# Optimization experiments

Measured on AMD Instinct MI355X. Metric: run time of the kernel, lower is better.

The kernel has to match this reference:

```python
import jax, jax.numpy as jnp
import numpy as np

C = 64  # channels fixed by module

def conv1x1(x, W, b):
    # x: [B,C,H,W], W: [C_out,C_in], b: [C_out]
    return jnp.einsum('bchw,oc->bohw', x, W) + b[None, :, None, None]

def setup_inputs() -> dict:
    key = jax.random.key(0)
    ks = jax.random.split(key, 16)
    B, H, W = 4, 64, 64
    inp = {
        'x_latter': jax.random.normal(ks[0], (B, C, H, W), jnp.float32),
        'x': jax.random.normal(ks[1], (B, C, H, W), jnp.float32),
    }
    scale = 1.0 / np.sqrt(C)
    names = ['high', 'low', 'value', 'e_conv', 'mid', 'latter']
    for i, n in enumerate(names):
        inp[f'W_{n}'] = jax.random.normal(ks[2 + 2 * i], (C, C), jnp.float32) * scale
        inp[f'b_{n}'] = jax.random.normal(ks[3 + 2 * i], (C,), jnp.float32) * 0.01
    return inp

def reference(x_latter, x, W_high, b_high, W_low, b_low, W_value, b_value,
              W_e_conv, b_e_conv, W_mid, b_mid, W_latter, b_latter):
    b, c, h, w = x_latter.shape
    hw = h * w
    # stage 1: channel-normalized spatial attention
    xl_hi = conv1x1(x_latter, W_high, b_high).reshape(b, c, hw)          # [b,c,hw]
    x_low = conv1x1(x, W_low, b_low).reshape(b, c, hw).transpose(0, 2, 1)  # [b,hw,c]
    p = jnp.einsum('bnc,bcm->bnm', x_low, xl_hi)                          # [b,hw,hw]
    p = jax.nn.softmax(p, axis=1)  # torch Softmax(dim=1) over first hw axis
    v = conv1x1(x, W_value, b_value).reshape(b, c, hw).transpose(0, 2, 1)  # [b,hw,c]
    e = jnp.einsum('bnm,bmc->bnc', p, v) + x_low                          # [b,hw,c]
    e = e.transpose(0, 2, 1).reshape(b, c, h, w)                          # [b,c,h,w]
    e = conv1x1(e, W_e_conv, b_e_conv).reshape(b, c, hw)                  # [b,c,hw]
    # stage 2: channel-channel attention
    xl2 = conv1x1(x_latter, W_latter, b_latter).reshape(b, c, hw).transpose(0, 2, 1)  # [b,hw,c]
    t = jnp.einsum('bcn,bnd->bcd', e, xl2)                                # [b,c,c]
    t = jax.nn.softmax(t, axis=1)
    x_mid = conv1x1(x, W_mid, b_mid).reshape(b, c, hw).transpose(0, 2, 1)  # [b,hw,c]
    out = jnp.einsum('bnc,bcd->bnd', x_mid, t)                            # [b,hw,c]
    return out.transpose(0, 2, 1).reshape(b, c, h, w)
```

## Files before the change

kernel.cpp:

```cpp
#include <hip/hip_runtime.h>
#include <math.h>

#define BATCH 4
#define CH 64
#define HW 4096

typedef __attribute__((ext_vector_type(8))) short short8;
typedef __attribute__((ext_vector_type(4))) float f32x4;
typedef __attribute__((ext_vector_type(4))) float float4v;

#define MFMA(a, b, c) __builtin_amdgcn_mfma_f32_16x16x32_bf16(a, b, c, 0, 0, 0)

__device__ __forceinline__ short f2bf(float f) {
    unsigned u = __builtin_bit_cast(unsigned, f);
    u += 0x7fffu + ((u >> 16) & 1u);
    return (short)(u >> 16);
}
__device__ __forceinline__ float bf2f(short s) {
    unsigned u = ((unsigned)(unsigned short)s) << 16;
    return __builtin_bit_cast(float, u);
}
__device__ __forceinline__ void gld16(const short* g, short* l) {
    __builtin_amdgcn_global_load_lds(
        (const __attribute__((address_space(1))) unsigned int*)g,
        (__attribute__((address_space(3))) unsigned int*)l, 16, 0, 0);
}

__global__ __launch_bounds__(256) void splitX(
    const float* __restrict__ x, const float* __restrict__ xl,
    short* __restrict__ XFh, short* __restrict__ XFl)
{
    int src = blockIdx.z, b = blockIdx.y, bx = blockIdx.x;
    const float* X = src ? xl : x;
    int t = threadIdx.x, wv = t >> 6, ln = t & 63;
    int nt = bx * 4 + wv;
    int n = (nt << 4) + (ln & 15);
    int g = ln >> 4;
    size_t sb = ((size_t)(src * BATCH + b) * 256 + nt) * 2;
    #pragma unroll
    for (int kt = 0; kt < 2; kt++) {
        short8 h, l;
        #pragma unroll
        for (int j = 0; j < 8; j++) {
            float v = X[(size_t)(b * 64 + kt * 32 + g * 8 + j) * HW + n];
            short hh = f2bf(v);
            h[j] = hh;
            l[j] = f2bf(v - bf2f(hh));
        }
        *(short8*)(XFh + (sb + kt) * 512 + (size_t)ln * 8) = h;
        *(short8*)(XFl + (sb + kt) * 512 + (size_t)ln * 8) = l;
    }
}

__global__ __launch_bounds__(256) void convm(
    const short* __restrict__ XFh, const short* __restrict__ XFl,
    const float* __restrict__ Wlow, const float* __restrict__ blow,
    const float* __restrict__ Wval, const float* __restrict__ bval,
    const float* __restrict__ Wmid, const float* __restrict__ bmid,
    const float* __restrict__ Wlat, const float* __restrict__ blat,
    const float* __restrict__ Whigh, const float* __restrict__ bhigh,
    float* __restrict__ XLOW, float* __restrict__ XMID, float* __restrict__ XL2,
    short* __restrict__ PAh, short* __restrict__ PAl,
    short* __restrict__ PBh, short* __restrict__ PBl,
    short* __restrict__ PVh, short* __restrict__ PVl)
{
    int mode = blockIdx.z, b = blockIdx.y, bx = blockIdx.x;
    const float* W; const float* bias; int src;
    switch (mode) {
        case 0:  W = Wlow;  bias = blow;  src = 0; break;
        case 1:  W = Wval;  bias = bval;  src = 0; break;
        case 2:  W = Wmid;  bias = bmid;  src = 0; break;
        case 3:  W = Wlat;  bias = blat;  src = 1; break;
        default: W = Whigh; bias = bhigh; src = 1; break;
    }
    int t = threadIdx.x, wv = t >> 6, ln = t & 63;
    int row = ln & 15, g = ln >> 4;

    short8 Wh[4][2], Wlo[4][2];
    #pragma unroll
    for (int ot = 0; ot < 4; ot++)
        #pragma unroll
        for (int kt = 0; kt < 2; kt++) {
            const float* wp = W + (ot * 16 + row) * 64 + kt * 32 + g * 8;
            short8 h, l;
            #pragma unroll
            for (int j = 0; j < 8; j++) {
                float v = wp[j];
                short hh = f2bf(v);
                h[j] = hh;
                l[j] = f2bf(v - bf2f(hh));
            }
            Wh[ot][kt] = h; Wlo[ot][kt] = l;
        }

    int nt = bx * 4 + wv;
    size_t xb = ((size_t)(src * BATCH + b) * 256 + nt) * 2;
    short8 Bh[2], Bl[2];
    #pragma unroll
    for (int kt = 0; kt < 2; kt++) {
        Bh[kt] = *(const short8*)(XFh + (xb + kt) * 512 + (size_t)ln * 8);
        Bl[kt] = *(const short8*)(XFl + (xb + kt) * 512 + (size_t)ln * 8);
    }

    f32x4 acc[4];
    #pragma unroll
    for (int ot = 0; ot < 4; ot++) {
        #pragma unroll
        for (int r = 0; r < 4; r++) acc[ot][r] = bias[ot * 16 + g * 4 + r];
    }
    #pragma unroll
    for (int ot = 0; ot < 4; ot++)
        #pragma unroll
        for (int kt = 0; kt < 2; kt++) {
            acc[ot] = MFMA(Wh[ot][kt], Bh[kt], acc[ot]);
            acc[ot] = MFMA(Wh[ot][kt], Bl[kt], acc[ot]);
            acc[ot] = MFMA(Wlo[ot][kt], Bh[kt], acc[ot]);
        }

    __shared__ float Ld[64][65];
    #pragma unroll
    for (int ot = 0; ot < 4; ot++)
        #pragma unroll
        for (int r = 0; r < 4; r++)
            Ld[wv * 16 + (ln & 15)][ot * 16 + g * 4 + r] = acc[ot][r];
    __syncthreads();

    int n0 = bx * 64;
    if (mode == 0 || mode == 2 || mode == 3) {
        float* outp = (mode == 0) ? XLOW : (mode == 2) ? XMID : XL2;
        int n = t >> 2, o0 = (t & 3) * 16;
        float vout[16];
        #pragma unroll
        for (int k = 0; k < 16; k++) vout[k] = Ld[n][o0 + k];
        float* gp = outp + ((size_t)b * HW + n0 + n) * 64 + o0;
        #pragma unroll
        for (int k = 0; k < 4; k++)
            *(float4v*)(gp + k * 4) = *(float4v*)(vout + k * 4);
    }
    if (mode == 0 || mode == 4) {
        short* Ph = (mode == 0) ? PAh : PBh;
        short* Pl = (mode == 0) ? PAl : PBl;
        #pragma unroll
        for (int kt = 0; kt < 2; kt++) {
            short8 h, l;
            #pragma unroll
            for (int j = 0; j < 8; j++) {
                float v = Ld[wv * 16 + (ln & 15)][kt * 32 + g * 8 + j];
                short hh = f2bf(v);
                h[j] = hh;
                l[j] = f2bf(v - bf2f(hh));
            }
            size_t blob = (((size_t)b * 256 + bx * 4 + wv) * 2 + kt) * 512 + (size_t)ln * 8;
            *(short8*)(Ph + blob) = h;
            *(short8*)(Pl + blob) = l;
        }
    }
    if (mode == 1) {
        int ktm_l = wv >> 1;
        int ct0 = (wv & 1) * 2;
        #pragma unroll
        for (int cc = 0; cc < 2; cc++) {
            int ct = ct0 + cc;
            int c = ct * 16 + (ln & 15);
            short8 h, l;
            #pragma unroll
            for (int j = 0; j < 8; j++) {
                float v = Ld[ktm_l * 32 + g * 8 + j][c];
                short hh = f2bf(v);
                h[j] = hh;
                l[j] = f2bf(v - bf2f(hh));
            }
            size_t blob = (((size_t)b * 128 + bx * 2 + ktm_l) * 4 + ct) * 512 + (size_t)ln * 8;
            *(short8*)(PVh + blob) = h;
            *(short8*)(PVl + blob) = l;
        }
    }
}

__global__ __launch_bounds__(256) void zpass(
    const short* __restrict__ PAh, const short* __restrict__ PAl,
    const short* __restrict__ PBh, const short* __restrict__ PBl,
    float* __restrict__ Zp)
{
    int b = blockIdx.z, nc = blockIdx.y, mchunk = blockIdx.x;
    int t = threadIdx.x, wv = t >> 6, ln = t & 63;
    short8 bh[4][2], bl[4][2];
    #pragma unroll
    for (int msub = 0; msub < 4; msub++)
        #pragma unroll
        for (int kt = 0; kt < 2; kt++) {
            size_t o = ((size_t)(b * 256 + mchunk * 4 + msub) * 2 + kt) * 512 + ln * 8;
            bh[msub][kt] = *(const short8*)(PBh + o);
            bl[msub][kt] = *(const short8*)(PBl + o);
        }
    float zacc[4] = {0.f, 0.f, 0.f, 0.f};
    for (int s = 0; s < 16; s++) {
        int nt = nc * 64 + s * 4 + wv;
        size_t ab = ((size_t)(b * 256 + nt) * 2) * 512 + ln * 8;
        short8 ah0 = *(const short8*)(PAh + ab);
        short8 ah1 = *(const short8*)(PAh + ab + 512);
        short8 al0 = *(const short8*)(PAl + ab);
        short8 al1 = *(const short8*)(PAl + ab + 512);
        #pragma unroll
        for (int msub = 0; msub < 4; msub++) {
            f32x4 acc = {0.f, 0.f, 0.f, 0.f};
            acc = MFMA(ah0, bh[msub][0], acc);
            acc = MFMA(ah1, bh[msub][1], acc);
            acc = MFMA(ah0, bl[msub][0], acc);
            acc = MFMA(ah1, bl[msub][1], acc);
            acc = MFMA(al0, bh[msub][0], acc);
            acc = MFMA(al1, bh[msub][1], acc);
            float z = __expf(acc[0]) + __expf(acc[1]) + __expf(acc[2]) + __expf(acc[3]);
            z += __shfl_xor(z, 16, 64);
            z += __shfl_xor(z, 32, 64);
            zacc[msub] += z;
        }
    }
    __shared__ float sZ[4][64];
    if (ln < 16) {
        #pragma unroll
        for (int msub = 0; msub < 4; msub++) sZ[wv][msub * 16 + ln] = zacc[msub];
    }
    __syncthreads();
    if (t < 64) {
        float z = sZ[0][t] + sZ[1][t] + sZ[2][t] + sZ[3][t];
        Zp[((size_t)(b * 4 + nc)) * 4096 + mchunk * 64 + t] = z;
    }
}

__global__ __launch_bounds__(256) void zmerge(
    const float* __restrict__ Zp, float* __restrict__ Zi)
{
    int gi = blockIdx.x * 256 + threadIdx.x;
    int b = gi >> 12, m = gi & 4095;
    float z = 0.f;
    #pragma unroll
    for (int nc2 = 0; nc2 < 4; nc2++) z += Zp[((size_t)(b * 4 + nc2)) * 4096 + m];
    Zi[gi] = 1.f / z;
}

__global__ __launch_bounds__(512) void epass3(
    const short* __restrict__ PAh, const short* __restrict__ PAl,
    const short* __restrict__ PBh, const short* __restrict__ PBl,
    const short* __restrict__ PVh, const short* __restrict__ PVl,
    const float* __restrict__ Zi, float* __restrict__ Ep)
{
    int b = blockIdx.z, mseg = blockIdx.y, nb = blockIdx.x;
    int t = threadIdx.x, wv = t >> 6, ln = t & 63;
    int lnm = ln & 15, lnr = ln >> 4;

    __shared__ __align__(16) short sB[2][2][4096];
    __shared__ __align__(16) short sV[2][2][4096];
    __shared__ __align__(16) short sW[8][2][2][2][512];
    __shared__ float sZi[1024];

    int nt = nb * 16 + wv * 2;
    short8 Ah[2][2], Al[2][2];
    #pragma unroll
    for (int rt = 0; rt < 2; rt++)
        #pragma unroll
        for (int kt = 0; kt < 2; kt++) {
            size_t base = ((size_t)(b * 256 + nt + rt) * 2 + kt) * 512 + ln * 8;
            Ah[rt][kt] = *(const short8*)(PAh + base);
            Al[rt][kt] = *(const short8*)(PAl + base);
        }
    sZi[t]       = Zi[b * 4096 + mseg * 1024 + t];
    sZi[t + 512] = Zi[b * 4096 + mseg * 1024 + t + 512];
    __syncthreads();

    f32x4 acc_e[2][4];
    #pragma unroll
    for (int rt = 0; rt < 2; rt++)
        #pragma unroll
        for (int ct = 0; ct < 4; ct++) acc_e[rt][ct] = (f32x4){0.f, 0.f, 0.f, 0.f};

    const int mc0 = mseg * 16;
    #define STAGE(bufi, ii) { \
        size_t bb = (size_t)b * 262144 + (size_t)(mc0 + (ii)) * 4096 + t * 8; \
        gld16(PBh + bb, &sB[bufi][0][wv * 512]); \
        gld16(PBl + bb, &sB[bufi][1][wv * 512]); \
        gld16(PVh + bb, &sV[bufi][0][wv * 512]); \
        gld16(PVl + bb, &sV[bufi][1][wv * 512]); }

    STAGE(0, 0);
    for (int i = 0; i < 16; i++) {
        int cur = i & 1;
        __builtin_amdgcn_s_barrier();
        if (i < 15) {
            STAGE(cur ^ 1, i + 1);
            asm volatile("s_waitcnt vmcnt(4)" ::: "memory");
        } else {
            asm volatile("s_waitcnt vmcnt(0)" ::: "memory");
        }
        __builtin_amdgcn_sched_barrier(0);

        #pragma unroll
        for (int msub = 0; msub < 4; msub++) {
            const short8 bh0 = *(const short8*)&sB[cur][0][(msub * 2 + 0) * 512 + ln * 8];
            const short8 bh1 = *(const short8*)&sB[cur][0][(msub * 2 + 1) * 512 + ln * 8];
            const short8 bl0 = *(const short8*)&sB[cur][1][(msub * 2 + 0) * 512 + ln * 8];
            const short8 bl1 = *(const short8*)&sB[cur][1][(msub * 2 + 1) * 512 + ln * 8];
            float zi = sZi[i * 64 + msub * 16 + lnm];
            int m = msub * 16 + lnm;
            int ktw = m >> 5, j = m & 7, g = (m >> 3) & 3;
            #pragma unroll
            for (int rt = 0; rt < 2; rt++) {
                f32x4 acc = {0.f, 0.f, 0.f, 0.f};
                acc = MFMA(Ah[rt][0], bh0, acc);
                acc = MFMA(Ah[rt][1], bh1, acc);
                acc = MFMA(Ah[rt][0], bl0, acc);
                acc = MFMA(Ah[rt][1], bl1, acc);
                acc = MFMA(Al[rt][0], bh0, acc);
                acc = MFMA(Al[rt][1], bh1, acc);
                #pragma unroll
                for (int r = 0; r < 4; r++) {
                    float w = __expf(acc[r]) * zi;
                    short wh = f2bf(w);
                    short wl2 = f2bf(w - bf2f(wh));
                    int lane2 = (lnr * 4 + r) + g * 16;
                    int slot = lane2 ^ (lane2 >> 3);
                    sW[wv][rt][0][ktw][slot * 8 + j] = wh;
                    sW[wv][rt][1][ktw][slot * 8 + j] = wl2;
                }
            }
        }
        int rslot = (ln ^ (ln >> 3)) * 8;
        #pragma unroll
        for (int kt = 0; kt < 2; kt++) {
            const short8 w0h = *(const short8*)&sW[wv][0][0][kt][rslot];
            const short8 w0l = *(const short8*)&sW[wv][0][1][kt][rslot];
            const short8 w1h = *(const short8*)&sW[wv][1][0][kt][rslot];
            const short8 w1l = *(const short8*)&sW[wv][1][1][kt][rslot];
            #pragma unroll
            for (int ct = 0; ct < 4; ct++) {
                const short8 vh = *(const short8*)&sV[cur][0][(kt * 4 + ct) * 512 + ln * 8];
                const short8 vl = *(const short8*)&sV[cur][1][(kt * 4 + ct) * 512 + ln * 8];
                acc_e[0][ct] = MFMA(w0h, vh, acc_e[0][ct]);
                acc_e[0][ct] = MFMA(w0h, vl, acc_e[0][ct]);
                acc_e[0][ct] = MFMA(w0l, vh, acc_e[0][ct]);
                acc_e[1][ct] = MFMA(w1h, vh, acc_e[1][ct]);
                acc_e[1][ct] = MFMA(w1h, vl, acc_e[1][ct]);
                acc_e[1][ct] = MFMA(w1l, vh, acc_e[1][ct]);
            }
        }
    }
    #undef STAGE

    float* ep = Ep + ((size_t)mseg * BATCH + b) * HW * 64;
    #pragma unroll
    for (int rt = 0; rt < 2; rt++) {
        int n0 = (nt + rt) * 16 + lnr * 4;
        #pragma unroll
        for (int ct = 0; ct < 4; ct++) {
            #pragma unroll
            for (int r = 0; r < 4; r++)
                ep[(size_t)(n0 + r) * 64 + ct * 16 + lnm] = acc_e[rt][ct][r];
        }
    }
}

__global__ __launch_bounds__(256) void econv5(
    const float* __restrict__ Ep, const float* __restrict__ XLOW,
    const float* __restrict__ W, const float* __restrict__ bias,
    float* __restrict__ E2)
{
    const size_t SEG = (size_t)BATCH * HW * 64;
    int b = blockIdx.y, n0 = blockIdx.x * 64, t = threadIdx.x;
    __shared__ float Wl[64][64];
    __shared__ float El[64][65];
    for (int i = t; i < 4096; i += 256) Wl[i >> 6][i & 63] = W[i];
    for (int i = t; i < 4096; i += 256) {
        int nl = i >> 6, c = i & 63;
        size_t idx = ((size_t)b * HW + n0 + nl) * 64 + c;
        El[nl][c] = XLOW[idx] + Ep[idx] + Ep[SEG + idx] + Ep[2 * SEG + idx] + Ep[3 * SEG + idx];
    }
    __syncthreads();
    int nl = t & 63, og = t >> 6;
    for (int k = 0; k < 16; k++) {
        int o = og * 16 + k;
        float a0 = bias[o], a1 = 0.f, a2 = 0.f, a3 = 0.f;
        #pragma unroll
        for (int c = 0; c < 64; c += 4) {
            a0 += Wl[o][c]     * El[nl][c];
            a1 += Wl[o][c + 1] * El[nl][c + 1];
            a2 += Wl[o][c + 2] * El[nl][c + 2];
            a3 += Wl[o][c + 3] * El[nl][c + 3];
        }
        E2[((size_t)b * 64 + o) * HW + n0 + nl] = (a0 + a1) + (a2 + a3);
    }
}

__global__ __launch_bounds__(1024) void tmat(
    const float* __restrict__ E2, const float* __restrict__ XL2, float* __restrict__ T)
{
    int b = blockIdx.y, c = blockIdx.x, t = threadIdx.x;
    int d = t & 63, nl = t >> 6;
    const float* e = E2 + ((size_t)b * 64 + c) * HW;
    const float* x2 = XL2 + (size_t)b * HW * 64;
    float a0 = 0.f, a1 = 0.f;
    #pragma unroll 4
    for (int k = 0; k < 256; k += 2) {
        int na = k * 16 + nl, nb2 = na + 16;
        a0 += e[na] * x2[(size_t)na * 64 + d];
        a1 += e[nb2] * x2[(size_t)nb2 * 64 + d];
    }
    __shared__ float red[16][64];
    red[nl][d] = a0 + a1;
    __syncthreads();
    if (t < 64) {
        float s = 0.f;
        #pragma unroll
        for (int j = 0; j < 16; j++) s += red[j][t];
        T[((size_t)b * 64 + c) * 64 + t] = s;
    }
}

__global__ __launch_bounds__(64) void softT(
    const float* __restrict__ T, float* __restrict__ Ts)
{
    int d = blockIdx.x, b = blockIdx.y, c = threadIdx.x;
    float v = T[((size_t)b * 64 + c) * 64 + d];
    float M = v;
    #pragma unroll
    for (int o = 32; o > 0; o >>= 1) M = fmaxf(M, __shfl_xor(M, o, 64));
    float ez = __expf(v - M);
    float Z = ez;
    #pragma unroll
    for (int o = 32; o > 0; o >>= 1) Z += __shfl_xor(Z, o, 64);
    Ts[((size_t)b * 64 + c) * 64 + d] = ez / Z;
}

__global__ __launch_bounds__(256) void outk(
    const float* __restrict__ XMID, const float* __restrict__ Ts, float* __restrict__ out)
{
    int b = blockIdx.y, n0 = blockIdx.x * 64, t = threadIdx.x;
    __shared__ float Xm[64][65];
    __shared__ float Tl[64][64];
    for (int i = t; i < 4096; i += 256) {
        int nl = i >> 6, c = i & 63;
        Xm[nl][c] = XMID[((size_t)b * HW + n0 + nl) * 64 + c];
    }
    for (int i = t; i < 4096; i += 256) Tl[i >> 6][i & 63] = Ts[(size_t)b * 4096 + i];
    __syncthreads();
    int nl = t & 63, dg = t >> 6;
    float accs[16];
    #pragma unroll
    for (int k = 0; k < 16; k++) accs[k] = 0.f;
    for (int c = 0; c < 64; c++) {
        float xv = Xm[nl][c];
        #pragma unroll
        for (int k = 0; k < 16; k++) accs[k] += xv * Tl[c][dg * 16 + k];
    }
    #pragma unroll
    for (int k = 0; k < 16; k++) {
        int d = dg * 16 + k;
        out[((size_t)b * 64 + d) * HW + n0 + nl] = accs[k];
    }
}

extern "C" void kernel_launch(void* const* d_in, const int* in_sizes, int n_in,
                              void* d_out, int out_size, void* d_ws, size_t ws_size,
                              hipStream_t stream)
{
    const float* x_latter = (const float*)d_in[0];
    const float* x        = (const float*)d_in[1];
    const float* W_high = (const float*)d_in[2];  const float* b_high = (const float*)d_in[3];
    const float* W_low  = (const float*)d_in[4];  const float* b_low  = (const float*)d_in[5];
    const float* W_val  = (const float*)d_in[6];  const float* b_val  = (const float*)d_in[7];
    const float* W_ec   = (const float*)d_in[8];  const float* b_ec   = (const float*)d_in[9];
    const float* W_mid  = (const float*)d_in[10]; const float* b_mid  = (const float*)d_in[11];
    const float* W_lat  = (const float*)d_in[12]; const float* b_lat  = (const float*)d_in[13];
    float* outp = (float*)d_out;

    const size_t MAT = (size_t)BATCH * CH * HW;
    float* ws = (float*)d_ws;
    size_t off = 0;
    float* XLOW = ws + off; off += MAT;
    float* XMID = ws + off; off += MAT;
    float* XL2  = ws + off; off += MAT;
    float* Ep   = ws + off; off += 4 * MAT;
    float* Zp   = ws + off; off += (size_t)BATCH * 4 * HW;
    float* Zic  = ws + off; off += (size_t)BATCH * HW;
    float* T    = ws + off; off += (size_t)BATCH * 64 * 64;
    float* Ts   = ws + off; off += (size_t)BATCH * 64 * 64;
    short* sp = (short*)(ws + off);
    short* PAh = sp; sp += MAT;
    short* PAl = sp; sp += MAT;
    short* PBh = sp; sp += MAT;
    short* PBl = sp; sp += MAT;
    short* PVh = sp; sp += MAT;
    short* PVl = sp; sp += MAT;
    float* E2  = (float*)PAh;
    short* XFh = (short*)Ep;
    short* XFl = XFh + 2 * BATCH * 262144;

    splitX<<<dim3(64, BATCH, 2), 256, 0, stream>>>(x, x_latter, XFh, XFl);
    convm<<<dim3(64, BATCH, 5), 256, 0, stream>>>(
        XFh, XFl, W_low, b_low, W_val, b_val, W_mid, b_mid, W_lat, b_lat,
        W_high, b_high, XLOW, XMID, XL2, PAh, PAl, PBh, PBl, PVh, PVl);
    zpass<<<dim3(64, 4, BATCH), 256, 0, stream>>>(PAh, PAl, PBh, PBl, Zp);
    zmerge<<<dim3(64), 256, 0, stream>>>(Zp, Zic);
    epass3<<<dim3(16, 4, BATCH), 512, 0, stream>>>(PAh, PAl, PBh, PBl, PVh, PVl, Zic, Ep);
    econv5<<<dim3(64, BATCH), 256, 0, stream>>>(Ep, XLOW, W_ec, b_ec, E2);
    tmat<<<dim3(64, BATCH), 1024, 0, stream>>>(E2, XL2, T);
    softT<<<dim3(64, BATCH), 64, 0, stream>>>(T, Ts);
    outk<<<dim3(64, BATCH), 256, 0, stream>>>(XMID, Ts, outp);
}
```

Measured before the change: 159.6 us.

## Drop LDS staging in epass, halve rows per wave, swizzle block order

The attention-weight pass no longer stages B and V tiles through LDS with async global-to-LDS double buffering. Each wave now handles one 16-row tile instead of two and reads B and V fragments straight from global memory. That relies on L2 reuse, plus an XCD-aware block-index swizzle that keeps blocks of one batch on the same L2. The z-pass gets the same swizzle and defers its cross-lane shuffle reduction to the end of the loop. This trades LDS pressure and barriers for higher occupancy, at the cost of redundant global loads, half the register reuse of B, and more blocks.

```diff
diff --git a/kernel.cpp b/kernel.cpp
--- a/kernel.cpp
+++ b/kernel.cpp
@@ -19,11 +19,6 @@
 __device__ __forceinline__ float bf2f(short s) {
     unsigned u = ((unsigned)(unsigned short)s) << 16;
     return __builtin_bit_cast(float, u);
-}
-__device__ __forceinline__ void gld16(const short* g, short* l) {
-    __builtin_amdgcn_global_load_lds(
-        (const __attribute__((address_space(1))) unsigned int*)g,
-        (__attribute__((address_space(3))) unsigned int*)l, 16, 0, 0);
 }
 
 __global__ __launch_bounds__(256) void splitX(
@@ -177,12 +172,14 @@
     }
 }
 
-__global__ __launch_bounds__(256) void zpass(
+__global__ __launch_bounds__(256) void zpass2(
     const short* __restrict__ PAh, const short* __restrict__ PAl,
     const short* __restrict__ PBh, const short* __restrict__ PBl,
     float* __restrict__ Zp)
 {
-    int b = blockIdx.z, nc = blockIdx.y, mchunk = blockIdx.x;
+    int bid = blockIdx.x;
+    int sw = (bid & 7) * 128 + (bid >> 3);
+    int mchunk = sw & 63, nc = (sw >> 6) & 3, b = sw >> 8;
     int t = threadIdx.x, wv = t >> 6, ln = t & 63;
     short8 bh[4][2], bl[4][2];
     #pragma unroll
@@ -210,11 +207,13 @@
             acc = MFMA(ah1, bl[msub][1], acc);
             acc = MFMA(al0, bh[msub][0], acc);
             acc = MFMA(al1, bh[msub][1], acc);
-            float z = __expf(acc[0]) + __expf(acc[1]) + __expf(acc[2]) + __expf(acc[3]);
-            z += __shfl_xor(z, 16, 64);
-            z += __shfl_xor(z, 32, 64);
-            zacc[msub] += z;
-        }
+            zacc[msub] += __expf(acc[0]) + __expf(acc[1]) + __expf(acc[2]) + __expf(acc[3]);
+        }
+    }
+    #pragma unroll
+    for (int msub = 0; msub < 4; msub++) {
+        zacc[msub] += __shfl_xor(zacc[msub], 16, 64);
+        zacc[msub] += __shfl_xor(zacc[msub], 32, 64);
     }
     __shared__ float sZ[4][64];
     if (ln < 16) {
@@ -239,123 +238,91 @@
     Zi[gi] = 1.f / z;
 }
 
-__global__ __launch_bounds__(512) void epass3(
+__global__ __launch_bounds__(512, 4) void epass4(
     const short* __restrict__ PAh, const short* __restrict__ PAl,
     const short* __restrict__ PBh, const short* __restrict__ PBl,
     const short* __restrict__ PVh, const short* __restrict__ PVl,
     const float* __restrict__ Zi, float* __restrict__ Ep)
 {
-    int b = blockIdx.z, mseg = blockIdx.y, nb = blockIdx.x;
+    int bid = blockIdx.x;
+    int sw = (bid & 7) * 64 + (bid >> 3);
+    int b = sw >> 7, mseg = (sw >> 5) & 3, nb = sw & 31;
     int t = threadIdx.x, wv = t >> 6, ln = t & 63;
     int lnm = ln & 15, lnr = ln >> 4;
 
-    __shared__ __align__(16) short sB[2][2][4096];
-    __shared__ __align__(16) short sV[2][2][4096];
-    __shared__ __align__(16) short sW[8][2][2][2][512];
+    __shared__ __align__(16) short sW[8][2][2][512];
     __shared__ float sZi[1024];
-
-    int nt = nb * 16 + wv * 2;
-    short8 Ah[2][2], Al[2][2];
-    #pragma unroll
-    for (int rt = 0; rt < 2; rt++)
-        #pragma unroll
-        for (int kt = 0; kt < 2; kt++) {
-            size_t base = ((size_t)(b * 256 + nt + rt) * 2 + kt) * 512 + ln * 8;
-            Ah[rt][kt] = *(const short8*)(PAh + base);
-            Al[rt][kt] = *(const short8*)(PAl + base);
-        }
     sZi[t]       = Zi[b * 4096 + mseg * 1024 + t];
-    sZi[t + 512] = Zi[b * 4096 + mseg * 1024 + t + 512];
-    __syncthreads();
-
-    f32x4 acc_e[2][4];
-    #pragma unroll
-    for (int rt = 0; rt < 2; rt++)
-        #pragma unroll
-        for (int ct = 0; ct < 4; ct++) acc_e[rt][ct] = (f32x4){0.f, 0.f, 0.f, 0.f};
-
-    const int mc0 = mseg * 16;
-    #define STAGE(bufi, ii) { \
-        size_t bb = (size_t)b * 262144 + (size_t)(mc0 + (ii)) * 4096 + t * 8; \
-        gld16(PBh + bb, &sB[bufi][0][wv * 512]); \
-        gld16(PBl + bb, &sB[bufi][1][wv * 512]); \
-        gld16(PVh + bb, &sV[bufi][0][wv * 512]); \
-        gld16(PVl + bb, &sV[bufi][1][wv * 512]); }
-
-    STAGE(0, 0);
+    sZi[t + 512] = Zi[b * 4096 + mseg * 1024 + 512 + t];
+    __syncthreads();
+
+    int nt = nb * 8 + wv;
+    short8 Ah[2], Al[2];
+    #pragma unroll
+    for (int kt = 0; kt < 2; kt++) {
+        size_t base = ((size_t)(b * 256 + nt) * 2 + kt) * 512 + ln * 8;
+        Ah[kt] = *(const short8*)(PAh + base);
+        Al[kt] = *(const short8*)(PAl + base);
+    }
+
+    f32x4 acc_e[4];
+    #pragma unroll
+    for (int ct = 0; ct < 4; ct++) acc_e[ct] = (f32x4){0.f, 0.f, 0.f, 0.f};
+
     for (int i = 0; i < 16; i++) {
-        int cur = i & 1;
-        __builtin_amdgcn_s_barrier();
-        if (i < 15) {
-            STAGE(cur ^ 1, i + 1);
-            asm volatile("s_waitcnt vmcnt(4)" ::: "memory");
-        } else {
-            asm volatile("s_waitcnt vmcnt(0)" ::: "memory");
-        }
-        __builtin_amdgcn_sched_barrier(0);
-
+        int mc = mseg * 16 + i;
         #pragma unroll
         for (int msub = 0; msub < 4; msub++) {
-            const short8 bh0 = *(const short8*)&sB[cur][0][(msub * 2 + 0) * 512 + ln * 8];
-            const short8 bh1 = *(const short8*)&sB[cur][0][(msub * 2 + 1) * 512 + ln * 8];
-            const short8 bl0 = *(const short8*)&sB[cur][1][(msub * 2 + 0) * 512 + ln * 8];
-            const short8 bl1 = *(const short8*)&sB[cur][1][(msub * 2 + 1) * 512 + ln * 8];
+            size_t o = ((size_t)(b * 256 + mc * 4 + msub) * 2) * 512 + ln * 8;
+            const short8 bh0 = *(const short8*)(PBh + o);
+            const short8 bh1 = *(const short8*)(PBh + o + 512);
+            const short8 bl0 = *(const short8*)(PBl + o);
+            const short8 bl1 = *(const short8*)(PBl + o + 512);
+            f32x4 acc = {0.f, 0.f, 0.f, 0.f};
+            acc = MFMA(Ah[0], bh0, acc);
+            acc = MFMA(Ah[1], bh1, acc);
+            acc = MFMA(Ah[0], bl0, acc);
+            acc = MFMA(Ah[1], bl1, acc);
+            acc = MFMA(Al[0], bh0, acc);
+            acc = MFMA(Al[1], bh1, acc);
             float zi = sZi[i * 64 + msub * 16 + lnm];
             int m = msub * 16 + lnm;
             int ktw = m >> 5, j = m & 7, g = (m >> 3) & 3;
             #pragma unroll
-            for (int rt = 0; rt < 2; rt++) {
-                f32x4 acc = {0.f, 0.f, 0.f, 0.f};
-                acc = MFMA(Ah[rt][0], bh0, acc);
-                acc = MFMA(Ah[rt][1], bh1, acc);
-                acc = MFMA(Ah[rt][0], bl0, acc);
-                acc = MFMA(Ah[rt][1], bl1, acc);
-                acc = MFMA(Al[rt][0], bh0, acc);
-                acc = MFMA(Al[rt][1], bh1, acc);
-                #pragma unroll
-                for (int r = 0; r < 4; r++) {
-                    float w = __expf(acc[r]) * zi;
-                    short wh = f2bf(w);
-                    short wl2 = f2bf(w - bf2f(wh));
-                    int lane2 = (lnr * 4 + r) + g * 16;
-                    int slot = lane2 ^ (lane2 >> 3);
-                    sW[wv][rt][0][ktw][slot * 8 + j] = wh;
-                    sW[wv][rt][1][ktw][slot * 8 + j] = wl2;
-                }
+            for (int r = 0; r < 4; r++) {
+                float w = __expf(acc[r]) * zi;
+                short wh = f2bf(w);
+                short wl2 = f2bf(w - bf2f(wh));
+                int lane2 = (lnr * 4 + r) + g * 16;
+                int slot = lane2 ^ (lane2 >> 3);
+                sW[wv][0][ktw][slot * 8 + j] = wh;
+                sW[wv][1][ktw][slot * 8 + j] = wl2;
             }
         }
         int rslot = (ln ^ (ln >> 3)) * 8;
         #pragma unroll
         for (int kt = 0; kt < 2; kt++) {
-            const short8 w0h = *(const short8*)&sW[wv][0][0][kt][rslot];
-            const short8 w0l = *(const short8*)&sW[wv][0][1][kt][rslot];
-            const short8 w1h = *(const short8*)&sW[wv][1][0][kt][rslot];
-            const short8 w1l = *(const short8*)&sW[wv][1][1][kt][rslot];
+            const short8 wh = *(const short8*)&sW[wv][0][kt][rslot];
+            const short8 wl = *(const short8*)&sW[wv][1][kt][rslot];
+            size_t vb = ((size_t)(b * 128 + mc * 2 + kt) * 4) * 512 + ln * 8;
             #pragma unroll
             for (int ct = 0; ct < 4; ct++) {
-                const short8 vh = *(const short8*)&sV[cur][0][(kt * 4 + ct) * 512 + ln * 8];
-                const short8 vl = *(const short8*)&sV[cur][1][(kt * 4 + ct) * 512 + ln * 8];
-                acc_e[0][ct] = MFMA(w0h, vh, acc_e[0][ct]);
-                acc_e[0][ct] = MFMA(w0h, vl, acc_e[0][ct]);
-                acc_e[0][ct] = MFMA(w0l, vh, acc_e[0][ct]);
-                acc_e[1][ct] = MFMA(w1h, vh, acc_e[1][ct]);
-                acc_e[1][ct] = MFMA(w1h, vl, acc_e[1][ct]);
-                acc_e[1][ct] = MFMA(w1l, vh, acc_e[1][ct]);
+                const short8 vh = *(const short8*)(PVh + vb + ct * 512);
+                const short8 vl = *(const short8*)(PVl + vb + ct * 512);
+                acc_e[ct] = MFMA(wh, vh, acc_e[ct]);
+                acc_e[ct] = MFMA(wh, vl, acc_e[ct]);
+                acc_e[ct] = MFMA(wl, vh, acc_e[ct]);
             }
         }
     }
-    #undef STAGE
 
     float* ep = Ep + ((size_t)mseg * BATCH + b) * HW * 64;
-    #pragma unroll
-    for (int rt = 0; rt < 2; rt++) {
-        int n0 = (nt + rt) * 16 + lnr * 4;
-        #pragma unroll
-        for (int ct = 0; ct < 4; ct++) {
-            #pragma unroll
-            for (int r = 0; r < 4; r++)
-                ep[(size_t)(n0 + r) * 64 + ct * 16 + lnm] = acc_e[rt][ct][r];
-        }
+    int n0 = nt * 16 + lnr * 4;
+    #pragma unroll
+    for (int ct = 0; ct < 4; ct++) {
+        #pragma unroll
+        for (int r = 0; r < 4; r++)
+            ep[(size_t)(n0 + r) * 64 + ct * 16 + lnm] = acc_e[ct][r];
     }
 }
 
@@ -498,9 +465,9 @@
     convm<<<dim3(64, BATCH, 5), 256, 0, stream>>>(
         XFh, XFl, W_low, b_low, W_val, b_val, W_mid, b_mid, W_lat, b_lat,
         W_high, b_high, XLOW, XMID, XL2, PAh, PAl, PBh, PBl, PVh, PVl);
-    zpass<<<dim3(64, 4, BATCH), 256, 0, stream>>>(PAh, PAl, PBh, PBl, Zp);
+    zpass2<<<dim3(1024), 256, 0, stream>>>(PAh, PAl, PBh, PBl, Zp);
     zmerge<<<dim3(64), 256, 0, stream>>>(Zp, Zic);
-    epass3<<<dim3(16, 4, BATCH), 512, 0, stream>>>(PAh, PAl, PBh, PBl, PVh, PVl, Zic, Ep);
+    epass4<<<dim3(512), 512, 0, stream>>>(PAh, PAl, PBh, PBl, PVh, PVl, Zic, Ep);
     econv5<<<dim3(64, BATCH), 256, 0, stream>>>(Ep, XLOW, W_ec, b_ec, E2);
     tmat<<<dim3(64, BATCH), 1024, 0, stream>>>(E2, XL2, T);
     softT<<<dim3(64, BATCH), 64, 0, stream>>>(T, Ts);
```

New measurement: 176.6 us. +10.6%, slower.

## Keep softmax weights in registers via swapped MFMA operands; swizzle block order

Applied to the files above, without the earlier changes.

The attention-weight MFMA in the E pass now swaps its operands, so each lane's accumulator rows line up with the A-operand layout of the next MFMA. The exp-weighted probabilities are then repacked into bf16 hi/lo fragments in registers, which removes the sW shared-memory round trip. The V tile packing in convm is permuted to match the new k ordering. Blocks shrink to 256 threads with a 1D grid swizzled across XCDs, and zpass defers its cross-lane shuffles until after the loop. The risks are higher register pressure and the correctness of the permuted layout.

```diff
diff --git a/kernel.cpp b/kernel.cpp
--- a/kernel.cpp
+++ b/kernel.cpp
@@ -165,7 +165,7 @@
             short8 h, l;
             #pragma unroll
             for (int j = 0; j < 8; j++) {
-                float v = Ld[ktm_l * 32 + g * 8 + j][c];
+                float v = Ld[(ktm_l * 2 + (j >> 2)) * 16 + g * 4 + (j & 3)][c];
                 short hh = f2bf(v);
                 h[j] = hh;
                 l[j] = f2bf(v - bf2f(hh));
@@ -177,12 +177,14 @@
     }
 }
 
-__global__ __launch_bounds__(256) void zpass(
+__global__ __launch_bounds__(256) void zpass2(
     const short* __restrict__ PAh, const short* __restrict__ PAl,
     const short* __restrict__ PBh, const short* __restrict__ PBl,
     float* __restrict__ Zp)
 {
-    int b = blockIdx.z, nc = blockIdx.y, mchunk = blockIdx.x;
+    int bid = blockIdx.x;
+    int sw = (bid & 7) * 128 + (bid >> 3);
+    int mchunk = sw & 63, nc = (sw >> 6) & 3, b = sw >> 8;
     int t = threadIdx.x, wv = t >> 6, ln = t & 63;
     short8 bh[4][2], bl[4][2];
     #pragma unroll
@@ -210,11 +212,13 @@
             acc = MFMA(ah1, bl[msub][1], acc);
             acc = MFMA(al0, bh[msub][0], acc);
             acc = MFMA(al1, bh[msub][1], acc);
-            float z = __expf(acc[0]) + __expf(acc[1]) + __expf(acc[2]) + __expf(acc[3]);
-            z += __shfl_xor(z, 16, 64);
-            z += __shfl_xor(z, 32, 64);
-            zacc[msub] += z;
-        }
+            zacc[msub] += __expf(acc[0]) + __expf(acc[1]) + __expf(acc[2]) + __expf(acc[3]);
+        }
+    }
+    #pragma unroll
+    for (int msub = 0; msub < 4; msub++) {
+        zacc[msub] += __shfl_xor(zacc[msub], 16, 64);
+        zacc[msub] += __shfl_xor(zacc[msub], 32, 64);
     }
     __shared__ float sZ[4][64];
     if (ln < 16) {
@@ -239,34 +243,35 @@
     Zi[gi] = 1.f / z;
 }
 
-__global__ __launch_bounds__(512) void epass3(
+__global__ __launch_bounds__(256) void epass5(
     const short* __restrict__ PAh, const short* __restrict__ PAl,
     const short* __restrict__ PBh, const short* __restrict__ PBl,
     const short* __restrict__ PVh, const short* __restrict__ PVl,
     const float* __restrict__ Zi, float* __restrict__ Ep)
 {
-    int b = blockIdx.z, mseg = blockIdx.y, nb = blockIdx.x;
+    int bid = blockIdx.x;
+    int sw = (bid & 7) * 64 + (bid >> 3);
+    int b = sw >> 7, mseg = (sw >> 5) & 3, nb = sw & 31;
     int t = threadIdx.x, wv = t >> 6, ln = t & 63;
     int lnm = ln & 15, lnr = ln >> 4;
 
     __shared__ __align__(16) short sB[2][2][4096];
     __shared__ __align__(16) short sV[2][2][4096];
-    __shared__ __align__(16) short sW[8][2][2][2][512];
     __shared__ float sZi[1024];
 
-    int nt = nb * 16 + wv * 2;
-    short8 Ah[2][2], Al[2][2];
+    for (int k = t; k < 1024; k += 256) sZi[k] = Zi[b * 4096 + mseg * 1024 + k];
+    __syncthreads();
+
+    short8 Lh[2][2], Ll[2][2];
     #pragma unroll
     for (int rt = 0; rt < 2; rt++)
         #pragma unroll
         for (int kt = 0; kt < 2; kt++) {
-            size_t base = ((size_t)(b * 256 + nt + rt) * 2 + kt) * 512 + ln * 8;
-            Ah[rt][kt] = *(const short8*)(PAh + base);
-            Al[rt][kt] = *(const short8*)(PAl + base);
-        }
-    sZi[t]       = Zi[b * 4096 + mseg * 1024 + t];
-    sZi[t + 512] = Zi[b * 4096 + mseg * 1024 + t + 512];
-    __syncthreads();
+            int nt = nb * 8 + wv * 2 + rt;
+            size_t base = ((size_t)(b * 256 + nt) * 2 + kt) * 512 + ln * 8;
+            Lh[rt][kt] = *(const short8*)(PAh + base);
+            Ll[rt][kt] = *(const short8*)(PAl + base);
+        }
 
     f32x4 acc_e[2][4];
     #pragma unroll
@@ -276,11 +281,15 @@
 
     const int mc0 = mseg * 16;
     #define STAGE(bufi, ii) { \
-        size_t bb = (size_t)b * 262144 + (size_t)(mc0 + (ii)) * 4096 + t * 8; \
-        gld16(PBh + bb, &sB[bufi][0][wv * 512]); \
-        gld16(PBl + bb, &sB[bufi][1][wv * 512]); \
-        gld16(PVh + bb, &sV[bufi][0][wv * 512]); \
-        gld16(PVl + bb, &sV[bufi][1][wv * 512]); }
+        size_t bb = (size_t)b * 262144 + (size_t)(mc0 + (ii)) * 4096; \
+        gld16(PBh + bb + t * 8,        &sB[bufi][0][wv * 512]); \
+        gld16(PBh + bb + 2048 + t * 8, &sB[bufi][0][2048 + wv * 512]); \
+        gld16(PBl + bb + t * 8,        &sB[bufi][1][wv * 512]); \
+        gld16(PBl + bb + 2048 + t * 8, &sB[bufi][1][2048 + wv * 512]); \
+        gld16(PVh + bb + t * 8,        &sV[bufi][0][wv * 512]); \
+        gld16(PVh + bb + 2048 + t * 8, &sV[bufi][0][2048 + wv * 512]); \
+        gld16(PVl + bb + t * 8,        &sV[bufi][1][wv * 512]); \
+        gld16(PVl + bb + 2048 + t * 8, &sV[bufi][1][2048 + wv * 512]); }
 
     STAGE(0, 0);
     for (int i = 0; i < 16; i++) {
@@ -288,59 +297,61 @@
         __builtin_amdgcn_s_barrier();
         if (i < 15) {
             STAGE(cur ^ 1, i + 1);
-            asm volatile("s_waitcnt vmcnt(4)" ::: "memory");
+            asm volatile("s_waitcnt vmcnt(8)" ::: "memory");
         } else {
             asm volatile("s_waitcnt vmcnt(0)" ::: "memory");
         }
         __builtin_amdgcn_sched_barrier(0);
 
+        f32x4 wf[2][4];
         #pragma unroll
         for (int msub = 0; msub < 4; msub++) {
             const short8 bh0 = *(const short8*)&sB[cur][0][(msub * 2 + 0) * 512 + ln * 8];
             const short8 bh1 = *(const short8*)&sB[cur][0][(msub * 2 + 1) * 512 + ln * 8];
             const short8 bl0 = *(const short8*)&sB[cur][1][(msub * 2 + 0) * 512 + ln * 8];
             const short8 bl1 = *(const short8*)&sB[cur][1][(msub * 2 + 1) * 512 + ln * 8];
-            float zi = sZi[i * 64 + msub * 16 + lnm];
-            int m = msub * 16 + lnm;
-            int ktw = m >> 5, j = m & 7, g = (m >> 3) & 3;
+            const f32x4 vz = *(const f32x4*)&sZi[i * 64 + msub * 16 + lnr * 4];
             #pragma unroll
             for (int rt = 0; rt < 2; rt++) {
                 f32x4 acc = {0.f, 0.f, 0.f, 0.f};
-                acc = MFMA(Ah[rt][0], bh0, acc);
-                acc = MFMA(Ah[rt][1], bh1, acc);
-                acc = MFMA(Ah[rt][0], bl0, acc);
-                acc = MFMA(Ah[rt][1], bl1, acc);
-                acc = MFMA(Al[rt][0], bh0, acc);
-                acc = MFMA(Al[rt][1], bh1, acc);
+                acc = MFMA(bh0, Lh[rt][0], acc);
+                acc = MFMA(bh1, Lh[rt][1], acc);
+                acc = MFMA(bh0, Ll[rt][0], acc);
+                acc = MFMA(bh1, Ll[rt][1], acc);
+                acc = MFMA(bl0, Lh[rt][0], acc);
+                acc = MFMA(bl1, Lh[rt][1], acc);
                 #pragma unroll
-                for (int r = 0; r < 4; r++) {
-                    float w = __expf(acc[r]) * zi;
-                    short wh = f2bf(w);
-                    short wl2 = f2bf(w - bf2f(wh));
-                    int lane2 = (lnr * 4 + r) + g * 16;
-                    int slot = lane2 ^ (lane2 >> 3);
-                    sW[wv][rt][0][ktw][slot * 8 + j] = wh;
-                    sW[wv][rt][1][ktw][slot * 8 + j] = wl2;
+                for (int r = 0; r < 4; r++)
+                    wf[rt][msub][r] = __expf(acc[r]) * vz[r];
+            }
+        }
+        short8 pah[2][2], pal[2][2];
+        #pragma unroll
+        for (int rt = 0; rt < 2; rt++)
+            #pragma unroll
+            for (int kt = 0; kt < 2; kt++) {
+                short8 h, l;
+                #pragma unroll
+                for (int j = 0; j < 8; j++) {
+                    float w = wf[rt][kt * 2 + (j >> 2)][j & 3];
+                    short hh = f2bf(w);
+                    h[j] = hh;
+                    l[j] = f2bf(w - bf2f(hh));
                 }
+                pah[rt][kt] = h; pal[rt][kt] = l;
             }
-        }
-        int rslot = (ln ^ (ln >> 3)) * 8;
         #pragma unroll
         for (int kt = 0; kt < 2; kt++) {
-            const short8 w0h = *(const short8*)&sW[wv][0][0][kt][rslot];
-            const short8 w0l = *(const short8*)&sW[wv][0][1][kt][rslot];
-            const short8 w1h = *(const short8*)&sW[wv][1][0][kt][rslot];
-            const short8 w1l = *(const short8*)&sW[wv][1][1][kt][rslot];
             #pragma unroll
             for (int ct = 0; ct < 4; ct++) {
                 const short8 vh = *(const short8*)&sV[cur][0][(kt * 4 + ct) * 512 + ln * 8];
                 const short8 vl = *(const short8*)&sV[cur][1][(kt * 4 + ct) * 512 + ln * 8];
-                acc_e[0][ct] = MFMA(w0h, vh, acc_e[0][ct]);
-                acc_e[0][ct] = MFMA(w0h, vl, acc_e[0][ct]);
-                acc_e[0][ct] = MFMA(w0l, vh, acc_e[0][ct]);
-                acc_e[1][ct] = MFMA(w1h, vh, acc_e[1][ct]);
-                acc_e[1][ct] = MFMA(w1h, vl, acc_e[1][ct]);
-                acc_e[1][ct] = MFMA(w1l, vh, acc_e[1][ct]);
+                acc_e[0][ct] = MFMA(pah[0][kt], vh, acc_e[0][ct]);
+                acc_e[0][ct] = MFMA(pah[0][kt], vl, acc_e[0][ct]);
+                acc_e[0][ct] = MFMA(pal[0][kt], vh, acc_e[0][ct]);
+                acc_e[1][ct] = MFMA(pah[1][kt], vh, acc_e[1][ct]);
+                acc_e[1][ct] = MFMA(pah[1][kt], vl, acc_e[1][ct]);
+                acc_e[1][ct] = MFMA(pal[1][kt], vh, acc_e[1][ct]);
             }
         }
     }
@@ -349,7 +360,7 @@
     float* ep = Ep + ((size_t)mseg * BATCH + b) * HW * 64;
     #pragma unroll
     for (int rt = 0; rt < 2; rt++) {
-        int n0 = (nt + rt) * 16 + lnr * 4;
+        int n0 = (nb * 8 + wv * 2 + rt) * 16 + lnr * 4;
         #pragma unroll
         for (int ct = 0; ct < 4; ct++) {
             #pragma unroll
@@ -498,9 +509,9 @@
     convm<<<dim3(64, BATCH, 5), 256, 0, stream>>>(
         XFh, XFl, W_low, b_low, W_val, b_val, W_mid, b_mid, W_lat, b_lat,
         W_high, b_high, XLOW, XMID, XL2, PAh, PAl, PBh, PBl, PVh, PVl);
-    zpass<<<dim3(64, 4, BATCH), 256, 0, stream>>>(PAh, PAl, PBh, PBl, Zp);
+    zpass2<<<dim3(1024), 256, 0, stream>>>(PAh, PAl, PBh, PBl, Zp);
     zmerge<<<dim3(64), 256, 0, stream>>>(Zp, Zic);
-    epass3<<<dim3(16, 4, BATCH), 512, 0, stream>>>(PAh, PAl, PBh, PBl, PVh, PVl, Zic, Ep);
+    epass5<<<dim3(512), 256, 0, stream>>>(PAh, PAl, PBh, PBl, PVh, PVl, Zic, Ep);
     econv5<<<dim3(64, BATCH), 256, 0, stream>>>(Ep, XLOW, W_ec, b_ec, E2);
     tmat<<<dim3(64, BATCH), 1024, 0, stream>>>(E2, XL2, T);
     softT<<<dim3(64, BATCH), 64, 0, stream>>>(T, Ts);
```

Measured after the change: 153.1 us. -4.1%, faster.
